# Kernel tuning notes

Measured on AMD Instinct MI355X. Metric: run time of the kernel, lower is better.

Reference implementation:

```python
import jax, jax.numpy as jnp
import numpy as np

B, S, DIM, H, HD = 2, 2048, 512, 8, 64
VD = DIM // H  # 64
QK = H * HD


def setup_inputs() -> dict:
    key = jax.random.key(0)
    k1, k2, k3, k4, k5 = jax.random.split(key, 5)
    x = jax.random.normal(k1, (B, S, DIM), dtype=jnp.float32)
    mask = jax.random.bernoulli(k2, 0.5, (B, S))
    # per-position rotation matrices, scaled to keep activations O(1)
    rotator = jax.random.normal(k3, (B, S, HD, HD), dtype=jnp.float32) / np.sqrt(HD)
    # torch Linear weights: [out_features, in_features], no bias
    W_trans = jax.random.normal(k4, (2 * QK + DIM, DIM), dtype=jnp.float32) / np.sqrt(DIM)
    W_o = jax.random.normal(k5, (DIM, DIM), dtype=jnp.float32) / np.sqrt(DIM)
    return {"x": x, "mask": mask, "rotator": rotator, "W_trans": W_trans, "W_o": W_o}


def _taylor_attention(qs, ks, vs, mask):
    # 2nd-order Taylor approximation of exp for softmax weights
    # qs/ks: [B,S,H,HD], vs: [B,S,H,VD], mask: [B,S] key mask
    scores = jnp.einsum('bqhd,bkhd->bhqk', qs, ks) / np.sqrt(HD)
    w = 1.0 + scores + 0.5 * scores * scores
    w = jnp.where(mask[:, None, None, :], w, 0.0)
    w = w / jnp.sum(w, axis=-1, keepdims=True)
    out = jnp.einsum('bhqk,bkhd->bqhd', w, vs)
    return out.reshape(out.shape[0], out.shape[1], -1)  # [B,S,DIM]


def reference(x, mask, rotator, W_trans, W_o):
    t = x @ W_trans.T  # [B,S,2*QK+DIM]
    qs = t[..., :QK].reshape(B, S, H, HD)
    ks = t[..., QK:2 * QK].reshape(B, S, H, HD)
    vs = t[..., 2 * QK:].reshape(B, S, H, VD)
    sel = mask[..., None, None]
    qs = jnp.where(sel, jnp.einsum('bsij,bshj->bshi', rotator, qs), qs)
    ks = jnp.where(sel, jnp.einsum('bsij,bshj->bshi', rotator, ks), ks)
    out = _taylor_attention(qs, ks, vs, mask)
    return out @ W_o.T
```

## Files before the change

### kernel.cpp

```cpp
#include <hip/hip_runtime.h>
#include <hip/hip_bf16.h>

#define B_    2
#define S_    2048
#define DIM_  512
#define H_    8
#define HD_   64
#define TOUT_ 1536
#define ROWS_ (B_ * S_)

typedef unsigned short ushort_t;
typedef __attribute__((ext_vector_type(8))) __bf16 bf16x8;
typedef __attribute__((ext_vector_type(4))) float floatx4;
typedef __attribute__((ext_vector_type(16))) float floatx16;

#define AS_GLB __attribute__((address_space(1)))
#define AS_LDS __attribute__((address_space(3)))

__device__ __forceinline__ float bf2f(unsigned int u) { return __uint_as_float(u << 16); }
__device__ __forceinline__ unsigned int f2bfu(float f) {
    unsigned u = __float_as_uint(f);
    return (u + 0x7fffu + ((u >> 16) & 1u)) >> 16;
}
__device__ __forceinline__ bf16x8 cvt8(const float* p) {
    float4 a = *reinterpret_cast<const float4*>(p);
    float4 b = *reinterpret_cast<const float4*>(p + 4);
    ushort_t o[8] = {(ushort_t)f2bfu(a.x), (ushort_t)f2bfu(a.y), (ushort_t)f2bfu(a.z), (ushort_t)f2bfu(a.w),
                     (ushort_t)f2bfu(b.x), (ushort_t)f2bfu(b.y), (ushort_t)f2bfu(b.z), (ushort_t)f2bfu(b.w)};
    return *reinterpret_cast<bf16x8*>(o);
}

__global__ void tmha_detect(const unsigned char* mb, int* flags) {
    __shared__ int s_bf, s_f, s_u8;
    int tid = threadIdx.x;
    if (tid == 0) { s_bf = 0; s_f = 0; s_u8 = 0; }
    __syncthreads();
    int cbf = 0, cf = 0, cu8 = 0;
    for (int i = tid; i < 4096; i += 256) {
        unsigned char v = mb[i];
        if (v == 0x3F || v == 0x80) {
            cf++;
            if ((i & 3) == 1) cbf++;
        } else if (v != 0 && (i & 3) != 0) {
            cu8++;
        }
    }
    atomicAdd(&s_bf, cbf); atomicAdd(&s_f, cf); atomicAdd(&s_u8, cu8);
    __syncthreads();
    if (tid == 0) {
        int mcls;
        if (s_bf > 0)      mcls = 2;
        else if (s_f > 0)  mcls = 3;
        else if (s_u8 > 0) mcls = 0;
        else               mcls = 1;
        flags[1] = mcls;
    }
}

__global__ void tmha_decode_mask(const unsigned char* mb, const int* flags, int* wm) {
    int i = blockIdx.x * 256 + threadIdx.x;
    if (i >= ROWS_) return;
    int cls = flags[1];
    int v;
    if (cls == 0)      v = (mb[i] != 0);
    else if (cls == 1) v = (reinterpret_cast<const int*>(mb)[i] != 0);
    else if (cls == 2) v = ((reinterpret_cast<const unsigned short*>(mb)[i] & 0x7fffu) != 0);
    else               v = ((reinterpret_cast<const unsigned int*>(mb)[i] & 0x7fffffffu) != 0);
    wm[i] = v;
}

__global__ __launch_bounds__(256) void cast_bf16(const float* __restrict__ src,
                                                 ushort_t* __restrict__ dst, int n4) {
    int i = blockIdx.x * 256 + threadIdx.x;
    if (i >= n4) return;
    float4 v = reinterpret_cast<const float4*>(src)[i];
    ushort_t o[4] = {(ushort_t)f2bfu(v.x), (ushort_t)f2bfu(v.y), (ushort_t)f2bfu(v.z), (ushort_t)f2bfu(v.w)};
    reinterpret_cast<uint2*>(dst)[i] = *reinterpret_cast<uint2*>(o);
}

template <int TM, int N, int K>
__global__ __launch_bounds__(256) void mfma_gemm_bt(const ushort_t* __restrict__ A,
                                                    const ushort_t* __restrict__ Bm,
                                                    float* __restrict__ C) {
    constexpr int FM = TM / 32;
    __shared__ __align__(16) ushort_t As[TM * 64];
    __shared__ __align__(16) ushort_t Bs[128 * 64];
    int tid = threadIdx.x;
    int lane = tid & 63;
    int wv = tid >> 6;
    int wm = wv >> 1, wn = wv & 1;
    int quad = lane >> 4;
    int mrow = lane & 15;
    int bx = blockIdx.x;
    int by = blockIdx.y;

    floatx4 acc[FM][4];
#pragma unroll
    for (int i = 0; i < FM; i++)
#pragma unroll
        for (int j = 0; j < 4; j++) acc[i][j] = (floatx4){0.f, 0.f, 0.f, 0.f};

    for (int k0 = 0; k0 < K; k0 += 64) {
#pragma unroll
        for (int t = 0; t < TM / 32; t++) {
            int p = (wv * (TM / 32) + t) * 64 + lane;
            int row = p >> 3, cp = p & 7;
            int gc = cp ^ (row & 7);
            const ushort_t* ga = A + (size_t)(by * TM + row) * K + k0 + gc * 8;
            __builtin_amdgcn_global_load_lds((const AS_GLB unsigned int*)ga,
                                             (AS_LDS unsigned int*)&As[(size_t)(wv * (TM / 32) + t) * 64 * 8],
                                             16, 0, 0);
        }
#pragma unroll
        for (int t = 0; t < 4; t++) {
            int p = (wv * 4 + t) * 64 + lane;
            int row = p >> 3, cp = p & 7;
            int gc = cp ^ (row & 7);
            const ushort_t* gb = Bm + (size_t)(bx * 128 + row) * K + k0 + gc * 8;
            __builtin_amdgcn_global_load_lds((const AS_GLB unsigned int*)gb,
                                             (AS_LDS unsigned int*)&Bs[(size_t)(wv * 4 + t) * 64 * 8],
                                             16, 0, 0);
        }
        __syncthreads();
#pragma unroll
        for (int ks = 0; ks < 64; ks += 32) {
            int c = (ks >> 3) + quad;
            bf16x8 af[FM], bf[4];
#pragma unroll
            for (int i = 0; i < FM; i++) {
                int row = wm * (TM / 2) + i * 16 + mrow;
                int pos = row * 8 + (c ^ (row & 7));
                af[i] = *reinterpret_cast<const bf16x8*>(&As[pos * 8]);
            }
#pragma unroll
            for (int j = 0; j < 4; j++) {
                int row = wn * 64 + j * 16 + mrow;
                int pos = row * 8 + (c ^ (row & 7));
                bf[j] = *reinterpret_cast<const bf16x8*>(&Bs[pos * 8]);
            }
#pragma unroll
            for (int i = 0; i < FM; i++)
#pragma unroll
                for (int j = 0; j < 4; j++)
                    acc[i][j] = __builtin_amdgcn_mfma_f32_16x16x32_bf16(af[i], bf[j], acc[i][j], 0, 0, 0);
        }
        __syncthreads();
    }

    int col0 = bx * 128 + wn * 64 + mrow;
    int row0 = by * TM + wm * (TM / 2) + quad * 4;
#pragma unroll
    for (int i = 0; i < FM; i++)
#pragma unroll
        for (int j = 0; j < 4; j++)
#pragma unroll
            for (int r = 0; r < 4; r++)
                C[(size_t)(row0 + i * 16 + r) * N + col0 + j * 16] = acc[i][j][r];
}

__global__ __launch_bounds__(256) void rot_qk_mfma(const float* __restrict__ t,
                                                   const float* __restrict__ rotG,
                                                   const int* __restrict__ wm,
                                                   ushort_t* __restrict__ Qb,
                                                   ushort_t* __restrict__ Kb) {
    int lane = threadIdx.x & 63;
    int wv = threadIdx.x >> 6;
    int row = blockIdx.x * 4 + wv;
    int b = row >> 11, s = row & 2047;
    int lm = lane & 15, quad = lane >> 4;
    const float* trow = t + (size_t)row * TOUT_;

    if (wm[row]) {
        bf16x8 af[2];
#pragma unroll
        for (int kc = 0; kc < 2; kc++)
            af[kc] = cvt8(trow + lm * 64 + kc * 32 + quad * 8);

        const float* R = rotG + (size_t)row * 4096;
        floatx4 dacc[4];
#pragma unroll
        for (int nb = 0; nb < 4; nb++) dacc[nb] = (floatx4){0.f, 0.f, 0.f, 0.f};
#pragma unroll
        for (int nb = 0; nb < 4; nb++)
#pragma unroll
            for (int kc = 0; kc < 2; kc++) {
                bf16x8 bfr = cvt8(R + (size_t)(nb * 16 + lm) * 64 + kc * 32 + quad * 8);
                dacc[nb] = __builtin_amdgcn_mfma_f32_16x16x32_bf16(af[kc], bfr, dacc[nb], 0, 0, 0);
            }
#pragma unroll
        for (int nb = 0; nb < 4; nb++)
#pragma unroll
            for (int r = 0; r < 4; r++) {
                int vec = quad * 4 + r;
                int h = vec & 7;
                ushort_t* dst = (vec >= 8 ? Kb : Qb);
                dst[((size_t)(b * 8 + h) * 2048 + s) * 64 + nb * 16 + lm] = (ushort_t)f2bfu(dacc[nb][r]);
            }
    } else {
#pragma unroll
        for (int nb = 0; nb < 4; nb++)
#pragma unroll
            for (int r = 0; r < 4; r++) {
                int vec = quad * 4 + r;
                int h = vec & 7;
                float v = trow[vec * 64 + nb * 16 + lm];
                ushort_t* dst = (vec >= 8 ? Kb : Qb);
                dst[((size_t)(b * 8 + h) * 2048 + s) * 64 + nb * 16 + lm] = (ushort_t)f2bfu(v);
            }
    }
}

__global__ __launch_bounds__(256) void prep_vt(const float* __restrict__ t,
                                               const int* __restrict__ wm,
                                               ushort_t* __restrict__ VtG) {
    __shared__ float tile[64][65];
    __shared__ float mrow[64];
    int st = blockIdx.x;
    int bh = blockIdx.y;
    int b = bh >> 3, h = bh & 7;
    int tid = threadIdx.x;
    if (tid < 64) mrow[tid] = wm[b * 2048 + st * 64 + tid] ? 1.0f : 0.0f;
#pragma unroll
    for (int i = 0; i < 4; i++) {
        int q = i * 256 + tid;
        int r = q >> 4, c4 = (q & 15) * 4;
        float4 v = *reinterpret_cast<const float4*>(
            t + (size_t)(b * 2048 + st * 64 + r) * TOUT_ + 1024 + h * 64 + c4);
        tile[r][c4] = v.x; tile[r][c4 + 1] = v.y; tile[r][c4 + 2] = v.z; tile[r][c4 + 3] = v.w;
    }
    __syncthreads();
#pragma unroll
    for (int i = 0; i < 8; i++) {
        int e = i * 256 + tid;
        int d = e >> 5, sl = (e & 31) * 2;
        float v0 = tile[sl][d] * mrow[sl];
        float v1 = tile[sl + 1][d] * mrow[sl + 1];
        unsigned int u = f2bfu(v0) | (f2bfu(v1) << 16);
        *reinterpret_cast<unsigned int*>(VtG + ((size_t)bh * 65 + d) * 2048 + st * 64 + sl) = u;
    }
    if (tid < 32) {
        int sl = tid * 2;
        unsigned m0 = mrow[sl]     != 0.f ? 0x3F80u : 0u;
        unsigned m1 = mrow[sl + 1] != 0.f ? 0x3F80u : 0u;
        *reinterpret_cast<unsigned int*>(VtG + ((size_t)bh * 65 + 64) * 2048 + st * 64 + sl) = m0 | (m1 << 16);
    }
}

__global__ __launch_bounds__(256, 3) void tmha_attn_mfma(const ushort_t* __restrict__ Qb,
                                                         const ushort_t* __restrict__ Kb,
                                                         const ushort_t* __restrict__ VtG,
                                                         float* __restrict__ numer,
                                                         float* __restrict__ den) {
    __shared__ __align__(16) ushort_t Ks[128 * 64];
    __shared__ __align__(16) ushort_t Vs[64 * 128];
    __shared__ __align__(16) ushort_t Ps[64 * 128];
    __shared__ __align__(16) ushort_t Ms[128];
    __shared__ __align__(16) ushort_t Zb[8];
    int tid = threadIdx.x;
    int lane = tid & 63;
    int wv = tid >> 6;
    int qg = wv >> 1, kg = wv & 1;
    int l31 = lane & 31, lhi = lane >> 5;
    int qt = blockIdx.x;
    int h = blockIdx.y;
    int z = blockIdx.z;
    int b = z >> 1, ks = z & 1;
    int bh = b * 8 + h;
    if (tid < 4) reinterpret_cast<unsigned int*>(Zb)[tid] = 0u;

    bf16x8 qf[4];
    {
        const ushort_t* qp = Qb + ((size_t)bh * 2048 + qt * 64 + qg * 32 + l31) * 64 + lhi * 8;
        qf[0] = *reinterpret_cast<const bf16x8*>(qp);
        qf[1] = *reinterpret_cast<const bf16x8*>(qp + 16);
        qf[2] = *reinterpret_cast<const bf16x8*>(qp + 32);
        qf[3] = *reinterpret_cast<const bf16x8*>(qp + 48);
    }

    floatx16 oacc[3];
#pragma unroll
    for (int nt = 0; nt < 3; nt++)
#pragma unroll
        for (int e = 0; e < 16; e++) oacc[nt][e] = 0.f;

    int q = qg * 32 + l31;

    for (int kt = ks * 1024; kt < ks * 1024 + 1024; kt += 128) {
#pragma unroll
        for (int t4 = 0; t4 < 4; t4++) {
            int p = (wv * 4 + t4) * 64 + lane;
            int row = p >> 3, cp = p & 7;
            int gc = cp ^ (row & 7);
            const ushort_t* g = Kb + ((size_t)bh * 2048 + kt + row) * 64 + gc * 8;
            __builtin_amdgcn_global_load_lds((const AS_GLB unsigned int*)g,
                                             (AS_LDS unsigned int*)&Ks[(size_t)(wv * 4 + t4) * 64 * 8],
                                             16, 0, 0);
        }
#pragma unroll
        for (int t4 = 0; t4 < 4; t4++) {
            int p = (wv * 4 + t4) * 64 + lane;
            int row = p >> 4, cp = p & 15;
            int gc = cp ^ (row & 15);
            const ushort_t* g = VtG + ((size_t)bh * 65 + row) * 2048 + kt + gc * 8;
            __builtin_amdgcn_global_load_lds((const AS_GLB unsigned int*)g,
                                             (AS_LDS unsigned int*)&Vs[(size_t)(wv * 4 + t4) * 64 * 8],
                                             16, 0, 0);
        }
        if (tid < 64) {
            reinterpret_cast<unsigned int*>(Ms)[tid] = *reinterpret_cast<const unsigned int*>(
                VtG + ((size_t)bh * 65 + 64) * 2048 + kt + tid * 2);
        }
        __syncthreads();

        floatx16 sacc[2];
#pragma unroll
        for (int mt = 0; mt < 2; mt++)
#pragma unroll
            for (int e = 0; e < 16; e++) sacc[mt][e] = 0.f;
#pragma unroll
        for (int kstep = 0; kstep < 4; kstep++) {
            int g = kstep * 2 + lhi;
#pragma unroll
            for (int mt = 0; mt < 2; mt++) {
                int row = kg * 64 + mt * 32 + l31;
                int pos = row * 8 + (g ^ (row & 7));
                bf16x8 kf = *reinterpret_cast<const bf16x8*>(&Ks[pos * 8]);
                sacc[mt] = __builtin_amdgcn_mfma_f32_32x32x16_bf16(kf, qf[kstep], sacc[mt], 0, 0, 0);
            }
        }

#pragma unroll
        for (int mt = 0; mt < 2; mt++)
#pragma unroll
            for (int gg = 0; gg < 4; gg++) {
                float w[4];
#pragma unroll
                for (int r = 0; r < 4; r++) {
                    float s = sacc[mt][gg * 4 + r];
                    w[r] = fmaf(s, fmaf(s, 0.0078125f, 0.125f), 1.0f);
                }
                int k0 = kg * 64 + mt * 32 + gg * 8 + lhi * 4;
                int g16 = k0 >> 3;
                int pos = q * 16 + (g16 ^ (q & 15));
                uint2 u;
                u.x = f2bfu(w[0]) | (f2bfu(w[1]) << 16);
                u.y = f2bfu(w[2]) | (f2bfu(w[3]) << 16);
                *reinterpret_cast<uint2*>(&Ps[pos * 8 + (k0 & 7)]) = u;
            }
        __syncthreads();

#pragma unroll
        for (int kstep = 0; kstep < 4; kstep++) {
            int gk = kg * 8 + kstep * 2 + lhi;
            int ppos = q * 16 + (gk ^ (q & 15));
            bf16x8 pa = *reinterpret_cast<const bf16x8*>(&Ps[ppos * 8]);
#pragma unroll
            for (int nt = 0; nt < 3; nt++) {
                int vrow = nt * 32 + l31;
                const ushort_t* vp;
                if (vrow < 64)       vp = &Vs[(vrow * 16 + (gk ^ (vrow & 15))) * 8];
                else if (vrow == 64) vp = &Ms[gk * 8];
                else                 vp = Zb;
                bf16x8 vb = *reinterpret_cast<const bf16x8*>(vp);
                oacc[nt] = __builtin_amdgcn_mfma_f32_32x32x16_bf16(pa, vb, oacc[nt], 0, 0, 0);
            }
        }
        __syncthreads();
    }

    int sidx = ks * 2 + kg;
    int qbase = b * 2048 + qt * 64 + qg * 32;
#pragma unroll
    for (int nt = 0; nt < 2; nt++)
#pragma unroll
        for (int gg = 0; gg < 4; gg++)
#pragma unroll
            for (int r = 0; r < 4; r++) {
                int qrow = qbase + r + 8 * gg + 4 * lhi;
                numer[((size_t)sidx * ROWS_ + qrow) * DIM_ + h * 64 + nt * 32 + l31] = oacc[nt][gg * 4 + r];
            }
    if (l31 == 0) {
#pragma unroll
        for (int gg = 0; gg < 4; gg++)
#pragma unroll
            for (int r = 0; r < 4; r++) {
                int qrow = qbase + r + 8 * gg + 4 * lhi;
                den[((size_t)sidx * ROWS_ + qrow) * 8 + h] = oacc[2][gg * 4 + r];
            }
    }
}

__global__ __launch_bounds__(256) void attn_combine(const float* __restrict__ numer,
                                                    const float* __restrict__ den,
                                                    ushort_t* __restrict__ attnAb) {
    int i = blockIdx.x * 256 + threadIdx.x;
    int row = i >> 7;
    int c4 = (i & 127) * 4;
    int h = c4 >> 6;
    float nx = 0.f, ny = 0.f, nz = 0.f, nw = 0.f, d = 0.f;
#pragma unroll
    for (int s = 0; s < 4; s++) {
        float4 n = *reinterpret_cast<const float4*>(&numer[((size_t)s * ROWS_ + row) * DIM_ + c4]);
        nx += n.x; ny += n.y; nz += n.z; nw += n.w;
        d += den[((size_t)s * ROWS_ + row) * 8 + h];
    }
    float inv = 1.0f / d;
    ushort_t o[4] = {(ushort_t)f2bfu(nx * inv), (ushort_t)f2bfu(ny * inv),
                     (ushort_t)f2bfu(nz * inv), (ushort_t)f2bfu(nw * inv)};
    *reinterpret_cast<uint2*>(&attnAb[(size_t)row * DIM_ + c4]) = *reinterpret_cast<uint2*>(o);
}

extern "C" void kernel_launch(void* const* d_in, const int* in_sizes, int n_in,
                              void* d_out, int out_size, void* d_ws, size_t ws_size,
                              hipStream_t stream) {
    (void)in_sizes; (void)n_in; (void)out_size; (void)ws_size;
    const float* x    = (const float*)d_in[0];
    const void*  mask = d_in[1];
    const float* rot  = (const float*)d_in[2];
    const float* Wt   = (const float*)d_in[3];
    const float* Wo   = (const float*)d_in[4];

    char* ws = (char*)d_ws;
    int* flags       = (int*)ws;
    int* wmask       = (int*)(ws + 64);
    float* t         = (float*)(ws + 32768);
    ushort_t* Xb     = (ushort_t*)(ws + 25198592);
    ushort_t* Wtb    = (ushort_t*)(ws + 29392896);
    ushort_t* Wob    = (ushort_t*)(ws + 30965760);
    ushort_t* Qb     = (ushort_t*)(ws + 31490048);
    ushort_t* Kb     = (ushort_t*)(ws + 35684352);
    ushort_t* VtG    = (ushort_t*)(ws + 39878656);
    ushort_t* attnAb = (ushort_t*)(ws + 44138496);
    float* numer     = (float*)(ws + 50331648);
    float* den       = (float*)(ws + 83886080);

    tmha_detect<<<1, 256, 0, stream>>>((const unsigned char*)mask, flags);
    tmha_decode_mask<<<16, 256, 0, stream>>>((const unsigned char*)mask, flags, wmask);

    cast_bf16<<<(ROWS_ * DIM_ / 4 + 255) / 256, 256, 0, stream>>>(x, Xb, ROWS_ * DIM_ / 4);
    cast_bf16<<<(TOUT_ * DIM_ / 4 + 255) / 256, 256, 0, stream>>>(Wt, Wtb, TOUT_ * DIM_ / 4);
    cast_bf16<<<(DIM_ * DIM_ / 4 + 255) / 256, 256, 0, stream>>>(Wo, Wob, DIM_ * DIM_ / 4);

    {
        dim3 grid(TOUT_ / 128, ROWS_ / 64);
        mfma_gemm_bt<64, TOUT_, DIM_><<<grid, 256, 0, stream>>>(Xb, Wtb, t);
    }

    rot_qk_mfma<<<ROWS_ / 4, 256, 0, stream>>>(t, rot, wmask, Qb, Kb);

    {
        dim3 grid(32, 16);
        prep_vt<<<grid, 256, 0, stream>>>(t, wmask, VtG);
    }

    {
        dim3 grid(32, 8, 4);
        tmha_attn_mfma<<<grid, 256, 0, stream>>>(Qb, Kb, VtG, numer, den);
    }
    attn_combine<<<(ROWS_ * 128) / 256, 256, 0, stream>>>(numer, den, attnAb);

    {
        dim3 grid(DIM_ / 128, ROWS_ / 64);
        mfma_gemm_bt<64, DIM_, DIM_><<<grid, 256, 0, stream>>>(attnAb, Wob, (float*)d_out);
    }
}
```

Baseline: 202.7 us.

## Fuse prep kernels, read K from global, reduce key halves in LDS

Merges mask detection with decoding, the three bf16 casts into one launch, and the QK rotation with V transpose into one kernel. In attention, K fragments are now read directly from global memory instead of staged in LDS, which drops the K-tile LDS buffer and one barrier per tile and raises occupancy to 4 blocks. The two key-group partial results are reduced through LDS before the write, halving numer/den traffic and the combine reads. Risks include uncoalesced global K reads and a possible race on Ps now that the barrier between writing and reading it is gone.

```diff
diff --git a/kernel.cpp b/kernel.cpp
--- a/kernel.cpp
+++ b/kernel.cpp
@@ -30,7 +30,8 @@
     return *reinterpret_cast<bf16x8*>(o);
 }
 
-__global__ void tmha_detect(const unsigned char* mb, int* flags) {
+__global__ __launch_bounds__(256) void detect_decode(const unsigned char* __restrict__ mb,
+                                                     int* __restrict__ wm) {
     __shared__ int s_bf, s_f, s_u8;
     int tid = threadIdx.x;
     if (tid == 0) { s_bf = 0; s_f = 0; s_u8 = 0; }
@@ -47,20 +48,13 @@
     }
     atomicAdd(&s_bf, cbf); atomicAdd(&s_f, cf); atomicAdd(&s_u8, cu8);
     __syncthreads();
-    if (tid == 0) {
-        int mcls;
-        if (s_bf > 0)      mcls = 2;
-        else if (s_f > 0)  mcls = 3;
-        else if (s_u8 > 0) mcls = 0;
-        else               mcls = 1;
-        flags[1] = mcls;
-    }
-}
-
-__global__ void tmha_decode_mask(const unsigned char* mb, const int* flags, int* wm) {
-    int i = blockIdx.x * 256 + threadIdx.x;
+    int cls;
+    if (s_bf > 0)      cls = 2;
+    else if (s_f > 0)  cls = 3;
+    else if (s_u8 > 0) cls = 0;
+    else               cls = 1;
+    int i = blockIdx.x * 256 + tid;
     if (i >= ROWS_) return;
-    int cls = flags[1];
     int v;
     if (cls == 0)      v = (mb[i] != 0);
     else if (cls == 1) v = (reinterpret_cast<const int*>(mb)[i] != 0);
@@ -69,13 +63,20 @@
     wm[i] = v;
 }
 
-__global__ __launch_bounds__(256) void cast_bf16(const float* __restrict__ src,
-                                                 ushort_t* __restrict__ dst, int n4) {
+__global__ __launch_bounds__(256) void cast_all(const float* __restrict__ x,
+                                                const float* __restrict__ Wt,
+                                                const float* __restrict__ Wo,
+                                                ushort_t* __restrict__ Xb,
+                                                ushort_t* __restrict__ Wtb,
+                                                ushort_t* __restrict__ Wob) {
     int i = blockIdx.x * 256 + threadIdx.x;
-    if (i >= n4) return;
-    float4 v = reinterpret_cast<const float4*>(src)[i];
+    const float* src; ushort_t* dst; int j;
+    if (i < 524288)       { src = x;  dst = Xb;  j = i; }
+    else if (i < 720896)  { src = Wt; dst = Wtb; j = i - 524288; }
+    else                  { src = Wo; dst = Wob; j = i - 720896; }
+    float4 v = reinterpret_cast<const float4*>(src)[j];
     ushort_t o[4] = {(ushort_t)f2bfu(v.x), (ushort_t)f2bfu(v.y), (ushort_t)f2bfu(v.z), (ushort_t)f2bfu(v.w)};
-    reinterpret_cast<uint2*>(dst)[i] = *reinterpret_cast<uint2*>(o);
+    reinterpret_cast<uint2*>(dst)[j] = *reinterpret_cast<uint2*>(o);
 }
 
 template <int TM, int N, int K>
@@ -158,104 +159,105 @@
                 C[(size_t)(row0 + i * 16 + r) * N + col0 + j * 16] = acc[i][j][r];
 }
 
-__global__ __launch_bounds__(256) void rot_qk_mfma(const float* __restrict__ t,
-                                                   const float* __restrict__ rotG,
-                                                   const int* __restrict__ wm,
-                                                   ushort_t* __restrict__ Qb,
-                                                   ushort_t* __restrict__ Kb) {
-    int lane = threadIdx.x & 63;
-    int wv = threadIdx.x >> 6;
-    int row = blockIdx.x * 4 + wv;
-    int b = row >> 11, s = row & 2047;
-    int lm = lane & 15, quad = lane >> 4;
-    const float* trow = t + (size_t)row * TOUT_;
-
-    if (wm[row]) {
-        bf16x8 af[2];
-#pragma unroll
-        for (int kc = 0; kc < 2; kc++)
-            af[kc] = cvt8(trow + lm * 64 + kc * 32 + quad * 8);
-
-        const float* R = rotG + (size_t)row * 4096;
-        floatx4 dacc[4];
-#pragma unroll
-        for (int nb = 0; nb < 4; nb++) dacc[nb] = (floatx4){0.f, 0.f, 0.f, 0.f};
-#pragma unroll
-        for (int nb = 0; nb < 4; nb++)
-#pragma unroll
-            for (int kc = 0; kc < 2; kc++) {
-                bf16x8 bfr = cvt8(R + (size_t)(nb * 16 + lm) * 64 + kc * 32 + quad * 8);
-                dacc[nb] = __builtin_amdgcn_mfma_f32_16x16x32_bf16(af[kc], bfr, dacc[nb], 0, 0, 0);
-            }
-#pragma unroll
-        for (int nb = 0; nb < 4; nb++)
-#pragma unroll
-            for (int r = 0; r < 4; r++) {
-                int vec = quad * 4 + r;
-                int h = vec & 7;
-                ushort_t* dst = (vec >= 8 ? Kb : Qb);
-                dst[((size_t)(b * 8 + h) * 2048 + s) * 64 + nb * 16 + lm] = (ushort_t)f2bfu(dacc[nb][r]);
-            }
-    } else {
-#pragma unroll
-        for (int nb = 0; nb < 4; nb++)
-#pragma unroll
-            for (int r = 0; r < 4; r++) {
-                int vec = quad * 4 + r;
-                int h = vec & 7;
-                float v = trow[vec * 64 + nb * 16 + lm];
-                ushort_t* dst = (vec >= 8 ? Kb : Qb);
-                dst[((size_t)(b * 8 + h) * 2048 + s) * 64 + nb * 16 + lm] = (ushort_t)f2bfu(v);
-            }
-    }
-}
-
-__global__ __launch_bounds__(256) void prep_vt(const float* __restrict__ t,
-                                               const int* __restrict__ wm,
-                                               ushort_t* __restrict__ VtG) {
+__global__ __launch_bounds__(256) void rot_prep(const float* __restrict__ t,
+                                                const float* __restrict__ rotG,
+                                                const int* __restrict__ wm,
+                                                ushort_t* __restrict__ Qb,
+                                                ushort_t* __restrict__ Kb,
+                                                ushort_t* __restrict__ VtG) {
     __shared__ float tile[64][65];
     __shared__ float mrow[64];
-    int st = blockIdx.x;
-    int bh = blockIdx.y;
-    int b = bh >> 3, h = bh & 7;
+    int bid = blockIdx.x;
     int tid = threadIdx.x;
-    if (tid < 64) mrow[tid] = wm[b * 2048 + st * 64 + tid] ? 1.0f : 0.0f;
-#pragma unroll
-    for (int i = 0; i < 4; i++) {
-        int q = i * 256 + tid;
-        int r = q >> 4, c4 = (q & 15) * 4;
-        float4 v = *reinterpret_cast<const float4*>(
-            t + (size_t)(b * 2048 + st * 64 + r) * TOUT_ + 1024 + h * 64 + c4);
-        tile[r][c4] = v.x; tile[r][c4 + 1] = v.y; tile[r][c4 + 2] = v.z; tile[r][c4 + 3] = v.w;
-    }
-    __syncthreads();
-#pragma unroll
-    for (int i = 0; i < 8; i++) {
-        int e = i * 256 + tid;
-        int d = e >> 5, sl = (e & 31) * 2;
-        float v0 = tile[sl][d] * mrow[sl];
-        float v1 = tile[sl + 1][d] * mrow[sl + 1];
-        unsigned int u = f2bfu(v0) | (f2bfu(v1) << 16);
-        *reinterpret_cast<unsigned int*>(VtG + ((size_t)bh * 65 + d) * 2048 + st * 64 + sl) = u;
-    }
-    if (tid < 32) {
-        int sl = tid * 2;
-        unsigned m0 = mrow[sl]     != 0.f ? 0x3F80u : 0u;
-        unsigned m1 = mrow[sl + 1] != 0.f ? 0x3F80u : 0u;
-        *reinterpret_cast<unsigned int*>(VtG + ((size_t)bh * 65 + 64) * 2048 + st * 64 + sl) = m0 | (m1 << 16);
-    }
-}
-
-__global__ __launch_bounds__(256, 3) void tmha_attn_mfma(const ushort_t* __restrict__ Qb,
+
+    if (bid < 1024) {
+        int lane = tid & 63;
+        int wv = tid >> 6;
+        int row = bid * 4 + wv;
+        int b = row >> 11, s = row & 2047;
+        int lm = lane & 15, quad = lane >> 4;
+        const float* trow = t + (size_t)row * TOUT_;
+
+        if (wm[row]) {
+            bf16x8 af[2];
+#pragma unroll
+            for (int kc = 0; kc < 2; kc++)
+                af[kc] = cvt8(trow + lm * 64 + kc * 32 + quad * 8);
+            const float* R = rotG + (size_t)row * 4096;
+            floatx4 dacc[4];
+#pragma unroll
+            for (int nb = 0; nb < 4; nb++) dacc[nb] = (floatx4){0.f, 0.f, 0.f, 0.f};
+#pragma unroll
+            for (int nb = 0; nb < 4; nb++)
+#pragma unroll
+                for (int kc = 0; kc < 2; kc++) {
+                    bf16x8 bfr = cvt8(R + (size_t)(nb * 16 + lm) * 64 + kc * 32 + quad * 8);
+                    dacc[nb] = __builtin_amdgcn_mfma_f32_16x16x32_bf16(af[kc], bfr, dacc[nb], 0, 0, 0);
+                }
+#pragma unroll
+            for (int nb = 0; nb < 4; nb++)
+#pragma unroll
+                for (int r = 0; r < 4; r++) {
+                    int vec = quad * 4 + r;
+                    int h = vec & 7;
+                    ushort_t* dst = (vec >= 8 ? Kb : Qb);
+                    dst[((size_t)(b * 8 + h) * 2048 + s) * 64 + nb * 16 + lm] = (ushort_t)f2bfu(dacc[nb][r]);
+                }
+        } else {
+#pragma unroll
+            for (int nb = 0; nb < 4; nb++)
+#pragma unroll
+                for (int r = 0; r < 4; r++) {
+                    int vec = quad * 4 + r;
+                    int h = vec & 7;
+                    float v = trow[vec * 64 + nb * 16 + lm];
+                    ushort_t* dst = (vec >= 8 ? Kb : Qb);
+                    dst[((size_t)(b * 8 + h) * 2048 + s) * 64 + nb * 16 + lm] = (ushort_t)f2bfu(v);
+                }
+        }
+    } else {
+        int r2 = bid - 1024;
+        int st = r2 & 31;
+        int bh = r2 >> 5;
+        int b = bh >> 3, h = bh & 7;
+        if (tid < 64) mrow[tid] = wm[b * 2048 + st * 64 + tid] ? 1.0f : 0.0f;
+#pragma unroll
+        for (int i = 0; i < 4; i++) {
+            int q = i * 256 + tid;
+            int r = q >> 4, c4 = (q & 15) * 4;
+            float4 v = *reinterpret_cast<const float4*>(
+                t + (size_t)(b * 2048 + st * 64 + r) * TOUT_ + 1024 + h * 64 + c4);
+            tile[r][c4] = v.x; tile[r][c4 + 1] = v.y; tile[r][c4 + 2] = v.z; tile[r][c4 + 3] = v.w;
+        }
+        __syncthreads();
+#pragma unroll
+        for (int i = 0; i < 8; i++) {
+            int e = i * 256 + tid;
+            int d = e >> 5, sl = (e & 31) * 2;
+            float v0 = tile[sl][d] * mrow[sl];
+            float v1 = tile[sl + 1][d] * mrow[sl + 1];
+            unsigned int u = f2bfu(v0) | (f2bfu(v1) << 16);
+            *reinterpret_cast<unsigned int*>(VtG + ((size_t)bh * 65 + d) * 2048 + st * 64 + sl) = u;
+        }
+        if (tid < 32) {
+            int sl = tid * 2;
+            unsigned m0 = mrow[sl]     != 0.f ? 0x3F80u : 0u;
+            unsigned m1 = mrow[sl + 1] != 0.f ? 0x3F80u : 0u;
+            *reinterpret_cast<unsigned int*>(VtG + ((size_t)bh * 65 + 64) * 2048 + st * 64 + sl) = m0 | (m1 << 16);
+        }
+    }
+}
+
+__global__ __launch_bounds__(256, 4) void tmha_attn_mfma(const ushort_t* __restrict__ Qb,
                                                          const ushort_t* __restrict__ Kb,
                                                          const ushort_t* __restrict__ VtG,
                                                          float* __restrict__ numer,
                                                          float* __restrict__ den) {
-    __shared__ __align__(16) ushort_t Ks[128 * 64];
-    __shared__ __align__(16) ushort_t Vs[64 * 128];
-    __shared__ __align__(16) ushort_t Ps[64 * 128];
-    __shared__ __align__(16) ushort_t Ms[128];
-    __shared__ __align__(16) ushort_t Zb[8];
+    __shared__ __align__(16) char smem[33040];
+    ushort_t* Vs = (ushort_t*)smem;
+    ushort_t* Ps = (ushort_t*)(smem + 16384);
+    ushort_t* Ms = (ushort_t*)(smem + 32768);
+    ushort_t* Zb = (ushort_t*)(smem + 33024);
     int tid = threadIdx.x;
     int lane = tid & 63;
     int wv = tid >> 6;
@@ -284,18 +286,10 @@
         for (int e = 0; e < 16; e++) oacc[nt][e] = 0.f;
 
     int q = qg * 32 + l31;
-
-    for (int kt = ks * 1024; kt < ks * 1024 + 1024; kt += 128) {
-#pragma unroll
-        for (int t4 = 0; t4 < 4; t4++) {
-            int p = (wv * 4 + t4) * 64 + lane;
-            int row = p >> 3, cp = p & 7;
-            int gc = cp ^ (row & 7);
-            const ushort_t* g = Kb + ((size_t)bh * 2048 + kt + row) * 64 + gc * 8;
-            __builtin_amdgcn_global_load_lds((const AS_GLB unsigned int*)g,
-                                             (AS_LDS unsigned int*)&Ks[(size_t)(wv * 4 + t4) * 64 * 8],
-                                             16, 0, 0);
-        }
+    const ushort_t* kbase = Kb + ((size_t)bh * 2048 + ks * 1024 + kg * 64 + l31) * 64 + lhi * 8;
+
+    for (int ti = 0; ti < 8; ti++) {
+        int kt = ks * 1024 + ti * 128;
 #pragma unroll
         for (int t4 = 0; t4 < 4; t4++) {
             int p = (wv * 4 + t4) * 64 + lane;
@@ -317,17 +311,14 @@
         for (int mt = 0; mt < 2; mt++)
 #pragma unroll
             for (int e = 0; e < 16; e++) sacc[mt][e] = 0.f;
-#pragma unroll
-        for (int kstep = 0; kstep < 4; kstep++) {
-            int g = kstep * 2 + lhi;
+        const ushort_t* kp = kbase + (size_t)ti * 128 * 64;
+#pragma unroll
+        for (int kstep = 0; kstep < 4; kstep++)
 #pragma unroll
             for (int mt = 0; mt < 2; mt++) {
-                int row = kg * 64 + mt * 32 + l31;
-                int pos = row * 8 + (g ^ (row & 7));
-                bf16x8 kf = *reinterpret_cast<const bf16x8*>(&Ks[pos * 8]);
+                bf16x8 kf = *reinterpret_cast<const bf16x8*>(kp + mt * 2048 + kstep * 16);
                 sacc[mt] = __builtin_amdgcn_mfma_f32_32x32x16_bf16(kf, qf[kstep], sacc[mt], 0, 0, 0);
             }
-        }
 
 #pragma unroll
         for (int mt = 0; mt < 2; mt++)
@@ -347,7 +338,6 @@
                 u.y = f2bfu(w[2]) | (f2bfu(w[3]) << 16);
                 *reinterpret_cast<uint2*>(&Ps[pos * 8 + (k0 & 7)]) = u;
             }
-        __syncthreads();
 
 #pragma unroll
         for (int kstep = 0; kstep < 4; kstep++) {
@@ -368,25 +358,44 @@
         __syncthreads();
     }
 
-    int sidx = ks * 2 + kg;
-    int qbase = b * 2048 + qt * 64 + qg * 32;
-#pragma unroll
-    for (int nt = 0; nt < 2; nt++)
-#pragma unroll
-        for (int gg = 0; gg < 4; gg++)
-#pragma unroll
-            for (int r = 0; r < 4; r++) {
-                int qrow = qbase + r + 8 * gg + 4 * lhi;
-                numer[((size_t)sidx * ROWS_ + qrow) * DIM_ + h * 64 + nt * 32 + l31] = oacc[nt][gg * 4 + r];
-            }
-    if (l31 == 0) {
-#pragma unroll
-        for (int gg = 0; gg < 4; gg++)
-#pragma unroll
-            for (int r = 0; r < 4; r++) {
-                int qrow = qbase + r + 8 * gg + 4 * lhi;
-                den[((size_t)sidx * ROWS_ + qrow) * 8 + h] = oacc[2][gg * 4 + r];
-            }
+    float* red = (float*)smem;
+    if (kg == 1) {
+        float* my = red + (qg * 64 + lane) * 52;
+#pragma unroll
+        for (int nt = 0; nt < 3; nt++)
+#pragma unroll
+            for (int g4 = 0; g4 < 4; g4++) {
+                float4 v = {oacc[nt][g4 * 4], oacc[nt][g4 * 4 + 1], oacc[nt][g4 * 4 + 2], oacc[nt][g4 * 4 + 3]};
+                *reinterpret_cast<float4*>(my + nt * 16 + g4 * 4) = v;
+            }
+    }
+    __syncthreads();
+    if (kg == 0) {
+        const float* pr = red + (qg * 64 + lane) * 52;
+#pragma unroll
+        for (int nt = 0; nt < 3; nt++)
+#pragma unroll
+            for (int e = 0; e < 16; e++) oacc[nt][e] += pr[nt * 16 + e];
+
+        int qbase = b * 2048 + qt * 64 + qg * 32;
+#pragma unroll
+        for (int nt = 0; nt < 2; nt++)
+#pragma unroll
+            for (int gg = 0; gg < 4; gg++)
+#pragma unroll
+                for (int r = 0; r < 4; r++) {
+                    int qrow = qbase + r + 8 * gg + 4 * lhi;
+                    numer[((size_t)ks * ROWS_ + qrow) * DIM_ + h * 64 + nt * 32 + l31] = oacc[nt][gg * 4 + r];
+                }
+        if (l31 == 0) {
+#pragma unroll
+            for (int gg = 0; gg < 4; gg++)
+#pragma unroll
+                for (int r = 0; r < 4; r++) {
+                    int qrow = qbase + r + 8 * gg + 4 * lhi;
+                    den[((size_t)ks * ROWS_ + qrow) * 8 + h] = oacc[2][gg * 4 + r];
+                }
+        }
     }
 }
 
@@ -397,16 +406,12 @@
     int row = i >> 7;
     int c4 = (i & 127) * 4;
     int h = c4 >> 6;
-    float nx = 0.f, ny = 0.f, nz = 0.f, nw = 0.f, d = 0.f;
-#pragma unroll
-    for (int s = 0; s < 4; s++) {
-        float4 n = *reinterpret_cast<const float4*>(&numer[((size_t)s * ROWS_ + row) * DIM_ + c4]);
-        nx += n.x; ny += n.y; nz += n.z; nw += n.w;
-        d += den[((size_t)s * ROWS_ + row) * 8 + h];
-    }
+    float4 n0 = *reinterpret_cast<const float4*>(&numer[(size_t)row * DIM_ + c4]);
+    float4 n1 = *reinterpret_cast<const float4*>(&numer[((size_t)ROWS_ + row) * DIM_ + c4]);
+    float d = den[(size_t)row * 8 + h] + den[((size_t)ROWS_ + row) * 8 + h];
     float inv = 1.0f / d;
-    ushort_t o[4] = {(ushort_t)f2bfu(nx * inv), (ushort_t)f2bfu(ny * inv),
-                     (ushort_t)f2bfu(nz * inv), (ushort_t)f2bfu(nw * inv)};
+    ushort_t o[4] = {(ushort_t)f2bfu((n0.x + n1.x) * inv), (ushort_t)f2bfu((n0.y + n1.y) * inv),
+                     (ushort_t)f2bfu((n0.z + n1.z) * inv), (ushort_t)f2bfu((n0.w + n1.w) * inv)};
     *reinterpret_cast<uint2*>(&attnAb[(size_t)row * DIM_ + c4]) = *reinterpret_cast<uint2*>(o);
 }
 
@@ -421,7 +426,6 @@
     const float* Wo   = (const float*)d_in[4];
 
     char* ws = (char*)d_ws;
-    int* flags       = (int*)ws;
     int* wmask       = (int*)(ws + 64);
     float* t         = (float*)(ws + 32768);
     ushort_t* Xb     = (ushort_t*)(ws + 25198592);
@@ -432,31 +436,24 @@
     ushort_t* VtG    = (ushort_t*)(ws + 39878656);
     ushort_t* attnAb = (ushort_t*)(ws + 44138496);
     float* numer     = (float*)(ws + 50331648);
-    float* den       = (float*)(ws + 83886080);
-
-    tmha_detect<<<1, 256, 0, stream>>>((const unsigned char*)mask, flags);
-    tmha_decode_mask<<<16, 256, 0, stream>>>((const unsigned char*)mask, flags, wmask);
-
-    cast_bf16<<<(ROWS_ * DIM_ / 4 + 255) / 256, 256, 0, stream>>>(x, Xb, ROWS_ * DIM_ / 4);
-    cast_bf16<<<(TOUT_ * DIM_ / 4 + 255) / 256, 256, 0, stream>>>(Wt, Wtb, TOUT_ * DIM_ / 4);
-    cast_bf16<<<(DIM_ * DIM_ / 4 + 255) / 256, 256, 0, stream>>>(Wo, Wob, DIM_ * DIM_ / 4);
+    float* den       = (float*)(ws + 67108864);
+
+    detect_decode<<<16, 256, 0, stream>>>((const unsigned char*)mask, wmask);
+
+    cast_all<<<3072, 256, 0, stream>>>(x, Wt, Wo, Xb, Wtb, Wob);
 
     {
         dim3 grid(TOUT_ / 128, ROWS_ / 64);
         mfma_gemm_bt<64, TOUT_, DIM_><<<grid, 256, 0, stream>>>(Xb, Wtb, t);
     }
 
-    rot_qk_mfma<<<ROWS_ / 4, 256, 0, stream>>>(t, rot, wmask, Qb, Kb);
-
-    {
-        dim3 grid(32, 16);
-        prep_vt<<<grid, 256, 0, stream>>>(t, wmask, VtG);
-    }
+    rot_prep<<<1536, 256, 0, stream>>>(t, rot, wmask, Qb, Kb, VtG);
 
     {
         dim3 grid(32, 8, 4);
         tmha_attn_mfma<<<grid, 256, 0, stream>>>(Qb, Kb, VtG, numer, den);
     }
+
     attn_combine<<<(ROWS_ * 128) / 256, 256, 0, stream>>>(numer, den, attnAb);
 
     {
```

Result: slower. 223.7 us (+10.3%).
